# Kernel optimization log

Measured on AMD Instinct MI355X. Metric: run time of the kernel, lower is better.

Reference implementation:

```python
import jax, jax.numpy as jnp
import numpy as np

B, D, F_UP, F_DOWN, C = 4096, 768, 12288, 12288, 256


def setup_inputs() -> dict:
    key = jax.random.key(0)
    ks = jax.random.split(key, 12)
    s = np.float32(1.0 / np.sqrt(D))
    return {
        'initial_acts': jax.random.normal(ks[0], (B, D), jnp.float32),
        'x_up': jax.random.normal(ks[1], (B, D), jnp.float32),
        'ln_scale': jax.random.uniform(ks[2], (B,), jnp.float32) + 0.5,
        'W_enc_up': jax.random.normal(ks[3], (F_UP, D), jnp.float32) * s,
        'b_enc_up': jax.random.normal(ks[4], (F_UP,), jnp.float32) * 0.01,
        'b_dec_up': jax.random.normal(ks[5], (D,), jnp.float32) * 0.01,
        'W_dec_up': jax.random.normal(ks[6], (D, F_UP), jnp.float32) * s,
        'W_enc_down': jax.random.normal(ks[7], (F_DOWN, D), jnp.float32) * s,
        'b_enc_down': jax.random.normal(ks[8], (F_DOWN,), jnp.float32) * 0.01,
        'b_dec_down': jax.random.normal(ks[9], (D,), jnp.float32) * 0.01,
        'W_dec_down': jax.random.normal(ks[10], (D, F_DOWN), jnp.float32) * s,
        'connections': jax.random.randint(ks[11], (F_DOWN, C), 0, F_UP, jnp.int64),
        'k_up': 64,
        'k_down': 64,
    }


def _topk_sparse(pre, k):
    # pre: [B, F] -> keep top-k per row, zeros elsewhere
    vals, idx = jax.lax.top_k(pre, k)
    rows = jnp.arange(pre.shape[0])[:, None]
    return jnp.zeros_like(pre).at[rows, idx].set(vals)


def _topk_encode(x, W_enc, b_enc, b_dec, k):
    # AutoEncoderTopK.encode: relu(encoder(x - b_dec)), then top-k sparsify
    pre = jax.nn.relu((x - b_dec) @ W_enc.T + b_enc)
    return _topk_sparse(pre, k)


def reference(initial_acts, x_up, ln_scale, W_enc_up, b_enc_up, b_dec_up,
              W_dec_up, W_enc_down, b_enc_down, b_dec_down, W_dec_down,
              connections, k_up, k_down):
    f_down, f_up = W_enc_down.shape[0], W_enc_up.shape[0]
    # upstream features (vanilla_forward -> features[up_name])
    feat_up = _topk_encode(x_up, W_enc_up, b_enc_up, b_dec_up, k_up)  # [B, F_up]
    # connection mask [F_down, F_up] from index tensor
    rows = jnp.arange(f_down)[:, None]
    mask = jnp.zeros((f_down, f_up), jnp.bool_).at[rows, connections].set(True)
    # get_pruned_contributions: masked virtual-weight matmul
    virtual_w = (W_enc_down @ W_dec_up) * mask                        # [F_down, F_up]
    contributions = feat_up @ virtual_w.T + (W_enc_down @ b_dec_up)   # [B, F_down]
    # get_initial_contributions + accumulate
    approx = initial_acts @ W_enc_down.T + contributions
    # layernorm scale, encoder bias, b_dec correction
    approx = approx / ln_scale[:, None] + b_enc_down - (W_enc_down @ b_dec_down)
    # downstream TopK + decode
    feat_down = _topk_sparse(approx, k_down)                          # [B, F_down]
    recon = feat_down @ W_dec_down.T + b_dec_down                     # [B, D]
    return recon
```

## Files before the change

### kernel.cpp

```cpp
#include <hip/hip_runtime.h>
#include <stdint.h>

#define B_    4096
#define D_    768
#define FUP   12288
#define FDN   12288
#define CONN  256
#define KTOP  64
#define CHUNK 1024
#define NCH   (B_ / CHUNK)
#define CH2   512
#define NCH2  (B_ / CH2)
#define PDW   1024
#define NPW   (FUP / PDW)

typedef short short8v __attribute__((ext_vector_type(8)));
typedef float f32x4  __attribute__((ext_vector_type(4)));


__device__ __forceinline__ unsigned fkey(float x) {
    unsigned u = __float_as_uint(x);
    return (u & 0x80000000u) ? ~u : (u | 0x80000000u);
}

__device__ void topk64_block(const float* vals, int n, int* gidx, float* gval,
                             unsigned* hist, int* scratch)
{
    const int tid = threadIdx.x;
    const int ln = tid & 63, wv = tid >> 6;
    if (tid == 0) { scratch[0] = KTOP; scratch[1] = 0; scratch[2] = 0; scratch[3] = 0; }
    for (int l = 24; l >= 0; l -= 8) {
        hist[tid] = 0;
        __syncthreads();
        unsigned prefix = (unsigned)scratch[1];
        int need = scratch[0];
        unsigned hm = (l == 24) ? 0u : (0xFFFFFFFFu << (l + 8));
        for (int i = tid; i < n; i += 256) {
            unsigned key = fkey(vals[i]);
            if ((key & hm) == (prefix & hm)) atomicAdd(&hist[(key >> l) & 255], 1u);
        }
        __syncthreads();
        unsigned hown = hist[tid];
        unsigned x = hown;
#pragma unroll
        for (int off = 1; off < 64; off <<= 1) {
            int sl = ln + off;
            unsigned v = __shfl(x, sl < 64 ? sl : ln);
            x += (sl < 64) ? v : 0u;
        }
        if (ln == 0) ((unsigned*)scratch)[4 + wv] = x;
        __syncthreads();
        unsigned offw = 0;
        for (int w2 = wv + 1; w2 < 4; ++w2) offw += ((unsigned*)scratch)[4 + w2];
        unsigned T = x + offw;
        unsigned S = T - hown;
        if (S < (unsigned)need && T >= (unsigned)need) {
            scratch[1] = (int)(prefix | ((unsigned)tid << l));
            scratch[0] = need - (int)S;
        }
        __syncthreads();
    }
    unsigned thresh = (unsigned)scratch[1];
    for (int i = tid; i < n; i += 256) {
        float v = vals[i];
        unsigned key = fkey(v);
        if (key > thresh) {
            int p = atomicAdd(&scratch[2], 1);
            gidx[p] = i; gval[p] = v;
        } else if (key == thresh) {
            int p = atomicAdd(&scratch[3], 1);
            if (p < 64) scratch[4 + p] = i;
        }
    }
    __syncthreads();
    if (tid == 0) {
        int cnt = scratch[2];
        int ne  = KTOP - cnt;
        int ec  = scratch[3] < 64 ? scratch[3] : 64;
        for (int a2 = 0; a2 < ne; ++a2) {
            int best = 0x7fffffff, bi = -1;
            for (int q = 0; q < ec; ++q) {
                int id = scratch[4 + q];
                if (id >= 0 && id < best) { best = id; bi = q; }
            }
            if (bi >= 0) {
                scratch[4 + bi] = -1;
                gidx[cnt + a2] = best; gval[cnt + a2] = vals[best];
            }
        }
    }
    __syncthreads();
}


__global__ void k_detect(const int* __restrict__ conn, int* mode) {
    if (blockIdx.x == 0 && threadIdx.x == 0) {
        int z = 1;
        for (int i = 1; i < 128; i += 2) z &= (conn[i] == 0);
        *mode = z;
    }
}

__device__ __forceinline__ int getconn(const int* c, size_t e, int mode) {
    return mode ? c[2 * e] : c[e];
}

__global__ void k_zero(unsigned* __restrict__ p, int n) {
    for (int i = blockIdx.x * blockDim.x + threadIdx.x; i < n;
         i += gridDim.x * blockDim.x)
        p[i] = 0u;
}

__global__ void k_transpose(const float* __restrict__ in, float* __restrict__ out,
                            int R, int Cc) {
    __shared__ float t[32][33];
    int x = blockIdx.x * 32 + threadIdx.x;
    int yb = blockIdx.y * 32;
    for (int j = threadIdx.y; j < 32; j += 8)
        t[j][threadIdx.x] = in[(size_t)(yb + j) * Cc + x];
    __syncthreads();
    int xo  = yb + threadIdx.x;
    int yb2 = blockIdx.x * 32;
    for (int j = threadIdx.y; j < 32; j += 8)
        out[(size_t)(yb2 + j) * R + xo] = t[threadIdx.x][j];
}

__global__ void k_precompute(const float* __restrict__ Wup, const float* __restrict__ Wdn,
                             const float* __restrict__ b_enc_up, const float* __restrict__ b_enc_down,
                             const float* __restrict__ b_dec_up, const float* __restrict__ b_dec_down,
                             float* __restrict__ bias_up, float* __restrict__ c_in,
                             float* __restrict__ c_out) {
    int wave = threadIdx.x >> 6, lane = threadIdx.x & 63;
    int f = blockIdx.x * 4 + wave;
    if (f >= FUP) return;
    const float* ru = Wup + (size_t)f * D_;
    const float* rd = Wdn + (size_t)f * D_;
    float s1 = 0.f, s2 = 0.f, s3 = 0.f;
    for (int d = lane; d < D_; d += 64) {
        float bu = b_dec_up[d], bd = b_dec_down[d];
        s1 += ru[d] * bu;
        float w = rd[d];
        s2 += w * bu;
        s3 += w * bd;
    }
    for (int m = 32; m; m >>= 1) {
        s1 += __shfl_xor(s1, m);
        s2 += __shfl_xor(s2, m);
        s3 += __shfl_xor(s3, m);
    }
    if (!lane) {
        bias_up[f] = b_enc_up[f] - s1;
        c_in[f]  = s2;
        c_out[f] = b_enc_down[f] - s3;
    }
}

__device__ __forceinline__ unsigned short bf16rne(float f) {
    unsigned u = __float_as_uint(f);
    unsigned r = u + 0x7FFFu + ((u >> 16) & 1u);
    return (unsigned short)(r >> 16);
}
__global__ __launch_bounds__(256) void k_split3(const float* __restrict__ in,
                                                unsigned short* __restrict__ out,
                                                int R) {
    const size_t plane = (size_t)R * D_;
    size_t base = ((size_t)blockIdx.x * 256 + threadIdx.x) * 8;
    float v[8];
    *(float4*)&v[0] = *(const float4*)(in + base);
    *(float4*)&v[4] = *(const float4*)(in + base + 4);
    unsigned short h[8], m[8], l[8];
#pragma unroll
    for (int i = 0; i < 8; ++i) {
        float f = v[i];
        unsigned short hb = bf16rne(f);
        float hf = __uint_as_float((unsigned)hb << 16);
        float r1 = f - hf;
        unsigned short mb = bf16rne(r1);
        float mf = __uint_as_float((unsigned)mb << 16);
        float r2 = r1 - mf;
        unsigned short lb = bf16rne(r2);
        h[i] = hb; m[i] = mb; l[i] = lb;
    }
    *(short8v*)(out + base)             = *(short8v*)h;
    *(short8v*)(out + plane + base)     = *(short8v*)m;
    *(short8v*)(out + 2 * plane + base) = *(short8v*)l;
}

#define GBM 128
#define GBN 128
#define GBK 32

__device__ __forceinline__ void gld16(const void* g, void* l) {
    __builtin_amdgcn_global_load_lds(
        (const __attribute__((address_space(1))) unsigned int*)g,
        (__attribute__((address_space(3))) unsigned int*)l, 16, 0, 0);
}

__global__ __launch_bounds__(256, 2) void k_gemm_mfma(
    const unsigned short* __restrict__ Asp, const unsigned short* __restrict__ Bsp,
    float* __restrict__ C, const float* __restrict__ bias,
    int M, int N, int doRelu)
{
    __shared__ __attribute__((aligned(16))) unsigned short L[3072 * 8];
    const int tid = threadIdx.x;
    const int nbx = gridDim.x;
    const int nwg = nbx * gridDim.y;
    int id = blockIdx.y * nbx + blockIdx.x;
    if ((nwg & 7) == 0) id = (id & 7) * (nwg >> 3) + (id >> 3);
    const int bm = (id / nbx) * GBM, bn = (id % nbx) * GBN;

    const int wid = tid >> 6, lane = tid & 63;
    const int wm = (wid >> 1) * 64, wn = (wid & 1) * 64;
    const int l15 = lane & 15, g4 = lane >> 4;
    const size_t psA = (size_t)M * D_, psB = (size_t)N * D_;

    const unsigned short* gsrc[12];
    unsigned short* ldst[12];
#pragma unroll
    for (int q2 = 0; q2 < 12; ++q2) {
        int s  = wid * 768 + q2 * 64 + lane;
        int isB = (s >= 1536);
        int sl = isB ? (s - 1536) : s;
        int p  = sl >> 9;
        int rem = sl & 511;
        int r  = rem >> 2;
        int cs = rem & 3;
        int c  = cs ^ ((r >> 1) & 3);
        const unsigned short* bp = isB ? Bsp : Asp;
        size_t ps = isB ? psB : psA;
        int row = (isB ? bn : bm) + r;
        gsrc[q2] = bp + (size_t)p * ps + (size_t)row * D_ + c * 8;
        ldst[q2] = L + (wid * 768 + q2 * 64) * 8;
    }
    const int fA = ((wm + l15) >> 1) & 3;
    const int fB = ((wn + l15) >> 1) & 3;
    const unsigned short* aB = L + (wm + l15) * 32 + ((g4 ^ fA) * 8);
    const unsigned short* bB = L + 1536 * 8 + (wn + l15) * 32 + ((g4 ^ fB) * 8);

    f32x4 acc[4][4] = {};
    for (int k0 = 0; k0 < D_; k0 += GBK) {
        __syncthreads();
#pragma unroll
        for (int q2 = 0; q2 < 12; ++q2)
            gld16(gsrc[q2] + k0, ldst[q2]);
        __syncthreads();
        short8v af[3][4], bf[3][4];
#pragma unroll
        for (int i = 0; i < 4; ++i)
#pragma unroll
            for (int p = 0; p < 3; ++p) {
                af[p][i] = *(const short8v*)(aB + p * 4096 + i * 512);
                bf[p][i] = *(const short8v*)(bB + p * 4096 + i * 512);
            }
#pragma unroll
        for (int i = 0; i < 4; ++i)
#pragma unroll
            for (int j = 0; j < 4; ++j) {
                acc[i][j] = __builtin_amdgcn_mfma_f32_16x16x32_bf16(af[0][i], bf[0][j], acc[i][j], 0, 0, 0);
                acc[i][j] = __builtin_amdgcn_mfma_f32_16x16x32_bf16(af[0][i], bf[1][j], acc[i][j], 0, 0, 0);
                acc[i][j] = __builtin_amdgcn_mfma_f32_16x16x32_bf16(af[1][i], bf[0][j], acc[i][j], 0, 0, 0);
                acc[i][j] = __builtin_amdgcn_mfma_f32_16x16x32_bf16(af[1][i], bf[1][j], acc[i][j], 0, 0, 0);
                acc[i][j] = __builtin_amdgcn_mfma_f32_16x16x32_bf16(af[0][i], bf[2][j], acc[i][j], 0, 0, 0);
                acc[i][j] = __builtin_amdgcn_mfma_f32_16x16x32_bf16(af[2][i], bf[0][j], acc[i][j], 0, 0, 0);
            }
    }
#pragma unroll
    for (int i = 0; i < 4; ++i) {
        int gr0 = bm + wm + i * 16 + (lane >> 4) * 4;
#pragma unroll
        for (int j = 0; j < 4; ++j) {
            int gc = bn + wn + j * 16 + l15;
            float bv = bias ? bias[gc] : 0.f;
#pragma unroll
            for (int q = 0; q < 4; ++q) {
                float v = acc[i][j][q] + bv;
                if (doRelu) v = fmaxf(v, 0.f);
                C[(size_t)(gr0 + q) * N + gc] = v;
            }
        }
    }
}

__global__ __launch_bounds__(256) void k_topk_up(const float* __restrict__ big,
                                                 int* __restrict__ up_idx,
                                                 float* __restrict__ up_val) {
    __shared__ __attribute__((aligned(16))) float row[FUP];
    __shared__ unsigned hist[256];
    __shared__ int scratch[68];
    int b = blockIdx.x;
    const float4* s4 = (const float4*)(big + (size_t)b * FUP);
    float4* r4 = (float4*)row;
    for (int i = threadIdx.x; i < FUP / 4; i += 256) r4[i] = s4[i];
    __syncthreads();
    topk64_block(row, FUP, up_idx + b * 64, up_val + b * 64, hist, scratch);
}

__global__ __launch_bounds__(256) void k_sortwin(
    const int* __restrict__ conn, const int* __restrict__ mode_p,
    unsigned short* __restrict__ ent_fu, unsigned char* __restrict__ ent_c,
    unsigned short* __restrict__ woff)
{
    __shared__ int crow[CONN];
    __shared__ int cnt[NPW + 1];
    __shared__ int base[NPW + 1];
    __shared__ int cur[NPW + 1];
    int fd = blockIdx.x, tid = threadIdx.x;
    int mode = *mode_p;
    crow[tid] = getconn(conn, (size_t)fd * CONN + tid, mode);
    if (tid <= NPW) cnt[tid] = 0;
    __syncthreads();
    int fu = crow[tid];
    bool dup = false;
    for (int q = 0; q < tid; ++q) dup |= (crow[q] == fu);
    int win = dup ? NPW : (fu / PDW);
    atomicAdd(&cnt[win], 1);
    __syncthreads();
    if (tid == 0) {
        int run = 0;
        for (int i = 0; i <= NPW; ++i) { base[i] = run; run += cnt[i]; }
    }
    __syncthreads();
    if (tid <= NPW) {
        woff[fd * (NPW + 2) + tid] = (unsigned short)base[tid];
        cur[tid] = base[tid];
    }
    if (tid == 0) woff[fd * (NPW + 2) + NPW + 1] = (unsigned short)CONN;
    __syncthreads();
    int pos = atomicAdd(&cur[win], 1);
    ent_fu[(size_t)fd * CONN + pos] = (unsigned short)fu;
    ent_c[(size_t)fd * CONN + pos]  = (unsigned char)tid;
}

__global__ __launch_bounds__(256) void k_pd2(
    const float* __restrict__ Wdn, const float* __restrict__ WduT,
    const unsigned short* __restrict__ ent_fu, const unsigned char* __restrict__ ent_c,
    const unsigned short* __restrict__ woff, float* __restrict__ pd)
{
    __shared__ __attribute__((aligned(16))) float wrow[D_];
    int fd = blockIdx.x, win = blockIdx.y, tid = threadIdx.x;
    int s = woff[fd * (NPW + 2) + win];
    int e = woff[fd * (NPW + 2) + win + 1];
    if (win == NPW) {
        for (int t = s + tid; t < e; t += 256)
            pd[(size_t)fd * CONN + ent_c[(size_t)fd * CONN + t]] = 0.f;
        return;
    }
    if (s == e) return;
    const float4* wsrc = (const float4*)(Wdn + (size_t)fd * D_);
    for (int i = tid; i < D_ / 4; i += 256) ((float4*)wrow)[i] = wsrc[i];
    __syncthreads();
    const int wave = tid >> 6, lane = tid & 63;
    const int grp = lane >> 4, gi = lane & 15;
    float4 wr[12];
#pragma unroll
    for (int j = 0; j < 12; ++j)
        wr[j] = *(const float4*)&wrow[gi * 4 + j * 64];
    for (int q = s + wave * 4; q < e; q += 16) {
        int idx = q + grp;
        bool act = idx < e;
        int idxc = act ? idx : (e - 1);
        int fu = ent_fu[(size_t)fd * CONN + idxc];
        const float* wu = WduT + (size_t)fu * D_;
        float s0 = 0.f, s1 = 0.f, s2 = 0.f, s3 = 0.f;
#pragma unroll
        for (int j = 0; j < 12; j += 4) {
            float4 u0 = *(const float4*)&wu[gi * 4 + (j + 0) * 64];
            float4 u1 = *(const float4*)&wu[gi * 4 + (j + 1) * 64];
            float4 u2 = *(const float4*)&wu[gi * 4 + (j + 2) * 64];
            float4 u3 = *(const float4*)&wu[gi * 4 + (j + 3) * 64];
            s0 = fmaf(u0.x, wr[j + 0].x, s0); s0 = fmaf(u0.y, wr[j + 0].y, s0);
            s0 = fmaf(u0.z, wr[j + 0].z, s0); s0 = fmaf(u0.w, wr[j + 0].w, s0);
            s1 = fmaf(u1.x, wr[j + 1].x, s1); s1 = fmaf(u1.y, wr[j + 1].y, s1);
            s1 = fmaf(u1.z, wr[j + 1].z, s1); s1 = fmaf(u1.w, wr[j + 1].w, s1);
            s2 = fmaf(u2.x, wr[j + 2].x, s2); s2 = fmaf(u2.y, wr[j + 2].y, s2);
            s2 = fmaf(u2.z, wr[j + 2].z, s2); s2 = fmaf(u2.w, wr[j + 2].w, s2);
            s3 = fmaf(u3.x, wr[j + 3].x, s3); s3 = fmaf(u3.y, wr[j + 3].y, s3);
            s3 = fmaf(u3.z, wr[j + 3].z, s3); s3 = fmaf(u3.w, wr[j + 3].w, s3);
        }
        float sacc = (s0 + s1) + (s2 + s3);
#pragma unroll
        for (int m = 1; m < 16; m <<= 1) sacc += __shfl_xor(sacc, m);
        if (act && gi == 0)
            pd[(size_t)fd * CONN + ent_c[(size_t)fd * CONN + idx]] = sacc;
    }
}

__global__ void k_hist(const int* __restrict__ conn, const int* __restrict__ mode_p,
                       unsigned* __restrict__ counts, int total) {
    int mode = *mode_p;
    for (int e = blockIdx.x * blockDim.x + threadIdx.x; e < total;
         e += gridDim.x * blockDim.x)
        atomicAdd(&counts[getconn(conn, (size_t)e, mode)], 1u);
}

__global__ void k_scan(const unsigned* __restrict__ counts,
                       unsigned* __restrict__ offsets, unsigned* __restrict__ cursor) {
    __shared__ unsigned sums[256];
    int tid = threadIdx.x;
    const int CH = FUP / 256;
    unsigned local = 0;
    for (int i = 0; i < CH; ++i) local += counts[tid * CH + i];
    sums[tid] = local;
    __syncthreads();
    for (int off = 1; off < 256; off <<= 1) {
        unsigned v = 0;
        if (tid >= off) v = sums[tid - off];
        __syncthreads();
        sums[tid] += v;
        __syncthreads();
    }
    unsigned run = (tid == 0) ? 0u : sums[tid - 1];
    for (int i = 0; i < CH; ++i) {
        int idx = tid * CH + i;
        offsets[idx] = run;
        cursor[idx]  = run;
        run += counts[idx];
    }
    if (tid == 255) offsets[FUP] = run;
}

__global__ void k_scatter(const int* __restrict__ conn, const int* __restrict__ mode_p,
                          const float* __restrict__ pd, unsigned* __restrict__ cursor,
                          unsigned short* __restrict__ rev_fd, float* __restrict__ rev_w,
                          int total) {
    int mode = *mode_p;
    for (int e = blockIdx.x * blockDim.x + threadIdx.x; e < total;
         e += gridDim.x * blockDim.x) {
        int fu = getconn(conn, (size_t)e, mode);
        unsigned pos = atomicAdd(&cursor[fu], 1u);
        rev_fd[pos] = (unsigned short)(e >> 8);
        rev_w[pos]  = pd[e];
    }
}

__global__ __launch_bounds__(256) void k_down(
    const float* __restrict__ big , const float* __restrict__ ln_scale,
    const float* __restrict__ c_in, const float* __restrict__ c_out,
    const int* __restrict__ up_idx, const float* __restrict__ up_val,
    const unsigned* __restrict__ offsets, const unsigned short* __restrict__ rev_fd,
    const float* __restrict__ rev_w, int* __restrict__ down_idx,
    float* __restrict__ down_val)
{
    __shared__ __attribute__((aligned(16))) float contrib[FDN];
    __shared__ unsigned hist[256];
    __shared__ int scratch[68];
    int b = blockIdx.x, tid = threadIdx.x;
    float4* c4 = (float4*)contrib;
    for (int i = tid; i < FDN / 4; i += 256) c4[i] = make_float4(0.f, 0.f, 0.f, 0.f);
    __syncthreads();
    for (int j = 0; j < KTOP; ++j) {
        int fu = up_idx[b * 64 + j];
        float v = up_val[b * 64 + j];
        unsigned s = offsets[fu], e = offsets[fu + 1];
        for (unsigned t = s + tid; t < e; t += 256)
            atomicAdd(&contrib[rev_fd[t]], v * rev_w[t]);
    }
    __syncthreads();
    float ls = ln_scale[b];
    const float* ap = big + (size_t)b * FDN;
    for (int i = tid; i < FDN; i += 256)
        contrib[i] = (ap[i] + contrib[i] + c_in[i]) / ls + c_out[i];
    __syncthreads();
    topk64_block(contrib, FDN, down_idx + b * 64, down_val + b * 64, hist, scratch);
}

__global__ __launch_bounds__(256) void k_decode(
    const int* __restrict__ down_idx, const float* __restrict__ down_val,
    const float* __restrict__ WddT, const float* __restrict__ b_dec_down,
    float* __restrict__ out)
{
    __shared__ int fidx[64];
    __shared__ float fval[64];
    int b = blockIdx.x, tid = threadIdx.x;
    if (tid < 64) { fidx[tid] = down_idx[b * 64 + tid]; fval[tid] = down_val[b * 64 + tid]; }
    __syncthreads();
    float a0 = b_dec_down[tid], a1 = b_dec_down[tid + 256], a2 = b_dec_down[tid + 512];
    for (int j = 0; j < 64; ++j) {
        const float* r = WddT + (size_t)fidx[j] * D_;
        float v = fval[j];
        a0 += v * r[tid];
        a1 += v * r[tid + 256];
        a2 += v * r[tid + 512];
    }
    float* o = out + (size_t)b * D_;
    o[tid] = a0; o[tid + 256] = a1; o[tid + 512] = a2;
}


extern "C" void kernel_launch(void* const* d_in, const int* in_sizes, int n_in,
                              void* d_out, int out_size, void* d_ws, size_t ws_size,
                              hipStream_t stream)
{
    const float* initial_acts = (const float*)d_in[0];
    const float* x_up         = (const float*)d_in[1];
    const float* ln_scale     = (const float*)d_in[2];
    const float* W_enc_up     = (const float*)d_in[3];
    const float* b_enc_up     = (const float*)d_in[4];
    const float* b_dec_up     = (const float*)d_in[5];
    const float* W_dec_up     = (const float*)d_in[6];
    const float* W_enc_down   = (const float*)d_in[7];
    const float* b_enc_down   = (const float*)d_in[8];
    const float* b_dec_down   = (const float*)d_in[9];
    const float* W_dec_down   = (const float*)d_in[10];
    const int*   conn         = (const int*)d_in[11];
    float* out = (float*)d_out;

    char* w = (char*)d_ws;
    float*          big      = (float*)(w);
    float*          pd       = (float*)(w);
    unsigned short* ent_fu   = (unsigned short*)(w + 12582912);
    unsigned char*  ent_c    = (unsigned char*) (w + 18874368);
    unsigned short* woff     = (unsigned short*)(w + 22020096);
    unsigned short* Bsplit   = (unsigned short*)(w + 50331648);
    float*          Wt       = (float*)(w + 50331648);
    float*          rev_w    = (float*)(w + 106954752);
    unsigned short* Asplit1  = (unsigned short*)(w + 106954752);
    unsigned short* rev_fd   = (unsigned short*)(w + 119537664);
    unsigned short* Asplit2  = (unsigned short*)(w + 125829120);
    int*            up_idx   = (int*)  (w + 128188416);
    float*          up_val   = (float*)(w + 129236992);
    int*            down_idx = (int*)  (w + 130285568);
    float*          down_val = (float*)(w + 131334144);
    unsigned*       offsets  = (unsigned*)(w + 132382720);
    unsigned*       cursor   = (unsigned*)(w + 132448256);
    unsigned*       counts   = (unsigned*)(w + 132513792);
    float*          bias_up  = (float*)(w + 132579328);
    float*          c_in     = (float*)(w + 132628480);
    float*          c_out    = (float*)(w + 132677632);
    int*            mode_p   = (int*)  (w + 132726784);

    const int total_conn = FDN * CONN;
    dim3 tb(32, 8);

    k_detect<<<1, 64, 0, stream>>>(conn, mode_p);
    k_precompute<<<FUP / 4, 256, 0, stream>>>(W_enc_up, W_enc_down, b_enc_up, b_enc_down,
                                              b_dec_up, b_dec_down, bias_up, c_in, c_out);
    k_split3<<<FUP * D_ / 2048, 256, 0, stream>>>(W_enc_up, Bsplit, FUP);
    for (int c = 0; c < NCH; ++c) {
        k_split3<<<CHUNK * D_ / 2048, 256, 0, stream>>>(x_up + (size_t)c * CHUNK * D_,
                                                        Asplit1, CHUNK);
        k_gemm_mfma<<<dim3(FUP / GBN, CHUNK / GBM), 256, 0, stream>>>(
            Asplit1, Bsplit, big, bias_up, CHUNK, FUP, 1);
        k_topk_up<<<CHUNK, 256, 0, stream>>>(big, up_idx + (size_t)c * CHUNK * 64,
                                             up_val + (size_t)c * CHUNK * 64);
    }
    k_transpose<<<dim3(FUP / 32, D_ / 32), tb, 0, stream>>>(W_dec_up, Wt, D_, FUP);
    k_sortwin<<<FDN, 256, 0, stream>>>(conn, mode_p, ent_fu, ent_c, woff);
    k_pd2<<<dim3(FDN, NPW + 1), 256, 0, stream>>>(W_enc_down, Wt, ent_fu, ent_c, woff, pd);
    k_zero<<<48, 256, 0, stream>>>(counts, FUP);
    k_hist<<<4096, 256, 0, stream>>>(conn, mode_p, counts, total_conn);
    k_scan<<<1, 256, 0, stream>>>(counts, offsets, cursor);
    k_scatter<<<4096, 256, 0, stream>>>(conn, mode_p, pd, cursor, rev_fd, rev_w, total_conn);
    k_split3<<<FDN * D_ / 2048, 256, 0, stream>>>(W_enc_down, Bsplit, FDN);
    for (int c = 0; c < NCH2; ++c) {
        k_split3<<<CH2 * D_ / 2048, 256, 0, stream>>>(initial_acts + (size_t)c * CH2 * D_,
                                                      Asplit2, CH2);
        k_gemm_mfma<<<dim3(FDN / GBN, CH2 / GBM), 256, 0, stream>>>(
            Asplit2, Bsplit, big, nullptr, CH2, FDN, 0);
        k_down<<<CH2, 256, 0, stream>>>(big, ln_scale + (size_t)c * CH2, c_in, c_out,
                                        up_idx + (size_t)c * CH2 * 64,
                                        up_val + (size_t)c * CH2 * 64,
                                        offsets, rev_fd, rev_w,
                                        down_idx + (size_t)c * CH2 * 64,
                                        down_val + (size_t)c * CH2 * 64);
    }
    k_transpose<<<dim3(FDN / 32, D_ / 32), tb, 0, stream>>>(W_dec_down, Wt, D_, FDN);
    k_decode<<<B_, 256, 0, stream>>>(down_idx, down_val, Wt, b_dec_down, out);
}
```

Baseline: 3.325 ms.

## Fuse activation bf16x3 split into GEMM A-tile load and enlarge down chunk

The GEMM kernel now reads fp32 activations directly, splits them into three bf16 planes in registers and writes them to LDS, with register prefetch of the next K slice. This removes the separate k_split3 launches and the Asplit buffer round trips through global memory. The down-stage chunk size grows from 512 to 1024 rows, halving the number of launches. The pd dot product also loses its four-way partial sums, which lengthens the FMA dependency chain. In exchange the GEMM main loop does more VALU work per K step, and its A tile now moves through registers instead of asynchronous direct-to-LDS loads.

```diff
diff --git a/kernel.cpp b/kernel.cpp
--- a/kernel.cpp
+++ b/kernel.cpp
@@ -9,8 +9,6 @@
 #define KTOP  64
 #define CHUNK 1024
 #define NCH   (B_ / CHUNK)
-#define CH2   512
-#define NCH2  (B_ / CH2)
 #define PDW   1024
 #define NPW   (FUP / PDW)
 
@@ -196,8 +194,8 @@
         (__attribute__((address_space(3))) unsigned int*)l, 16, 0, 0);
 }
 
-__global__ __launch_bounds__(256, 2) void k_gemm_mfma(
-    const unsigned short* __restrict__ Asp, const unsigned short* __restrict__ Bsp,
+__global__ __launch_bounds__(256, 2) void k_gemm_mfma2(
+    const float* __restrict__ Afp, const unsigned short* __restrict__ Bsp,
     float* __restrict__ C, const float* __restrict__ bias,
     int M, int N, int doRelu)
 {
@@ -212,38 +210,71 @@
     const int wid = tid >> 6, lane = tid & 63;
     const int wm = (wid >> 1) * 64, wn = (wid & 1) * 64;
     const int l15 = lane & 15, g4 = lane >> 4;
-    const size_t psA = (size_t)M * D_, psB = (size_t)N * D_;
-
-    const unsigned short* gsrc[12];
-    unsigned short* ldst[12];
-#pragma unroll
-    for (int q2 = 0; q2 < 12; ++q2) {
-        int s  = wid * 768 + q2 * 64 + lane;
-        int isB = (s >= 1536);
-        int sl = isB ? (s - 1536) : s;
+    const size_t psB = (size_t)N * D_;
+
+    const unsigned short* gsrcB[6];
+    unsigned short* ldstB[6];
+#pragma unroll
+    for (int q2 = 0; q2 < 6; ++q2) {
+        int s  = 1536 + wid * 384 + q2 * 64 + lane;
+        int sl = s - 1536;
         int p  = sl >> 9;
         int rem = sl & 511;
         int r  = rem >> 2;
         int cs = rem & 3;
         int c  = cs ^ ((r >> 1) & 3);
-        const unsigned short* bp = isB ? Bsp : Asp;
-        size_t ps = isB ? psB : psA;
-        int row = (isB ? bn : bm) + r;
-        gsrc[q2] = bp + (size_t)p * ps + (size_t)row * D_ + c * 8;
-        ldst[q2] = L + (wid * 768 + q2 * 64) * 8;
-    }
+        gsrcB[q2] = Bsp + (size_t)p * psB + (size_t)(bn + r) * D_ + c * 8;
+        ldstB[q2] = L + (1536 + wid * 384 + q2 * 64) * 8;
+    }
+    const int ar = tid >> 1, ah2 = tid & 1;
+    const float* aptr = Afp + (size_t)(bm + ar) * D_ + ah2 * 16;
+    const int fR = (ar >> 1) & 3;
+    unsigned short* aw[3][2];
+#pragma unroll
+    for (int p = 0; p < 3; ++p)
+#pragma unroll
+        for (int cc = 0; cc < 2; ++cc)
+            aw[p][cc] = L + (p * 512 + ar * 4 + ((2 * ah2 + cc) ^ fR)) * 8;
+
     const int fA = ((wm + l15) >> 1) & 3;
     const int fB = ((wn + l15) >> 1) & 3;
     const unsigned short* aB = L + (wm + l15) * 32 + ((g4 ^ fA) * 8);
     const unsigned short* bB = L + 1536 * 8 + (wn + l15) * 32 + ((g4 ^ fB) * 8);
 
+    float a0[16];
+#pragma unroll
+    for (int j = 0; j < 4; ++j)
+        *(float4*)&a0[4 * j] = *(const float4*)(aptr + 4 * j);
+
     f32x4 acc[4][4] = {};
     for (int k0 = 0; k0 < D_; k0 += GBK) {
         __syncthreads();
 #pragma unroll
-        for (int q2 = 0; q2 < 12; ++q2)
-            gld16(gsrc[q2] + k0, ldst[q2]);
-        __syncthreads();
+        for (int q2 = 0; q2 < 6; ++q2)
+            gld16(gsrcB[q2] + k0, ldstB[q2]);
+        unsigned short hh_[16], mm_[16], ll_[16];
+#pragma unroll
+        for (int i = 0; i < 16; ++i) {
+            float f = a0[i];
+            unsigned short hb = bf16rne(f);
+            float hf = __uint_as_float((unsigned)hb << 16);
+            float r1 = f - hf;
+            unsigned short mb = bf16rne(r1);
+            float mf = __uint_as_float((unsigned)mb << 16);
+            unsigned short lb = bf16rne(r1 - mf);
+            hh_[i] = hb; mm_[i] = mb; ll_[i] = lb;
+        }
+#pragma unroll
+        for (int cc = 0; cc < 2; ++cc) {
+            *(short8v*)aw[0][cc] = *(const short8v*)&hh_[cc * 8];
+            *(short8v*)aw[1][cc] = *(const short8v*)&mm_[cc * 8];
+            *(short8v*)aw[2][cc] = *(const short8v*)&ll_[cc * 8];
+        }
+        __syncthreads();
+        int kn = (k0 + GBK < D_) ? (k0 + GBK) : k0;
+#pragma unroll
+        for (int j = 0; j < 4; ++j)
+            *(float4*)&a0[4 * j] = *(const float4*)(aptr + kn + 4 * j);
         short8v af[3][4], bf[3][4];
 #pragma unroll
         for (int i = 0; i < 4; ++i)
@@ -361,23 +392,15 @@
         int idxc = act ? idx : (e - 1);
         int fu = ent_fu[(size_t)fd * CONN + idxc];
         const float* wu = WduT + (size_t)fu * D_;
-        float s0 = 0.f, s1 = 0.f, s2 = 0.f, s3 = 0.f;
-#pragma unroll
-        for (int j = 0; j < 12; j += 4) {
-            float4 u0 = *(const float4*)&wu[gi * 4 + (j + 0) * 64];
-            float4 u1 = *(const float4*)&wu[gi * 4 + (j + 1) * 64];
-            float4 u2 = *(const float4*)&wu[gi * 4 + (j + 2) * 64];
-            float4 u3 = *(const float4*)&wu[gi * 4 + (j + 3) * 64];
-            s0 = fmaf(u0.x, wr[j + 0].x, s0); s0 = fmaf(u0.y, wr[j + 0].y, s0);
-            s0 = fmaf(u0.z, wr[j + 0].z, s0); s0 = fmaf(u0.w, wr[j + 0].w, s0);
-            s1 = fmaf(u1.x, wr[j + 1].x, s1); s1 = fmaf(u1.y, wr[j + 1].y, s1);
-            s1 = fmaf(u1.z, wr[j + 1].z, s1); s1 = fmaf(u1.w, wr[j + 1].w, s1);
-            s2 = fmaf(u2.x, wr[j + 2].x, s2); s2 = fmaf(u2.y, wr[j + 2].y, s2);
-            s2 = fmaf(u2.z, wr[j + 2].z, s2); s2 = fmaf(u2.w, wr[j + 2].w, s2);
-            s3 = fmaf(u3.x, wr[j + 3].x, s3); s3 = fmaf(u3.y, wr[j + 3].y, s3);
-            s3 = fmaf(u3.z, wr[j + 3].z, s3); s3 = fmaf(u3.w, wr[j + 3].w, s3);
-        }
-        float sacc = (s0 + s1) + (s2 + s3);
+        float sacc = 0.f;
+#pragma unroll
+        for (int j = 0; j < 12; ++j) {
+            float4 u = *(const float4*)&wu[gi * 4 + j * 64];
+            sacc = fmaf(u.x, wr[j].x, sacc);
+            sacc = fmaf(u.y, wr[j].y, sacc);
+            sacc = fmaf(u.z, wr[j].z, sacc);
+            sacc = fmaf(u.w, wr[j].w, sacc);
+        }
 #pragma unroll
         for (int m = 1; m < 16; m <<= 1) sacc += __shfl_xor(sacc, m);
         if (act && gi == 0)
@@ -514,20 +537,18 @@
     unsigned short* Bsplit   = (unsigned short*)(w + 50331648);
     float*          Wt       = (float*)(w + 50331648);
     float*          rev_w    = (float*)(w + 106954752);
-    unsigned short* Asplit1  = (unsigned short*)(w + 106954752);
     unsigned short* rev_fd   = (unsigned short*)(w + 119537664);
-    unsigned short* Asplit2  = (unsigned short*)(w + 125829120);
-    int*            up_idx   = (int*)  (w + 128188416);
-    float*          up_val   = (float*)(w + 129236992);
-    int*            down_idx = (int*)  (w + 130285568);
-    float*          down_val = (float*)(w + 131334144);
-    unsigned*       offsets  = (unsigned*)(w + 132382720);
-    unsigned*       cursor   = (unsigned*)(w + 132448256);
-    unsigned*       counts   = (unsigned*)(w + 132513792);
-    float*          bias_up  = (float*)(w + 132579328);
-    float*          c_in     = (float*)(w + 132628480);
-    float*          c_out    = (float*)(w + 132677632);
-    int*            mode_p   = (int*)  (w + 132726784);
+    int*            up_idx   = (int*)  (w + 125829120);
+    float*          up_val   = (float*)(w + 126877696);
+    int*            down_idx = (int*)  (w + 127926272);
+    float*          down_val = (float*)(w + 128974848);
+    unsigned*       offsets  = (unsigned*)(w + 130023424);
+    unsigned*       cursor   = (unsigned*)(w + 130088960);
+    unsigned*       counts   = (unsigned*)(w + 130154496);
+    float*          bias_up  = (float*)(w + 130220032);
+    float*          c_in     = (float*)(w + 130269184);
+    float*          c_out    = (float*)(w + 130318336);
+    int*            mode_p   = (int*)  (w + 130367488);
 
     const int total_conn = FDN * CONN;
     dim3 tb(32, 8);
@@ -537,10 +558,8 @@
                                               b_dec_up, b_dec_down, bias_up, c_in, c_out);
     k_split3<<<FUP * D_ / 2048, 256, 0, stream>>>(W_enc_up, Bsplit, FUP);
     for (int c = 0; c < NCH; ++c) {
-        k_split3<<<CHUNK * D_ / 2048, 256, 0, stream>>>(x_up + (size_t)c * CHUNK * D_,
-                                                        Asplit1, CHUNK);
-        k_gemm_mfma<<<dim3(FUP / GBN, CHUNK / GBM), 256, 0, stream>>>(
-            Asplit1, Bsplit, big, bias_up, CHUNK, FUP, 1);
+        k_gemm_mfma2<<<dim3(FUP / GBN, CHUNK / GBM), 256, 0, stream>>>(
+            x_up + (size_t)c * CHUNK * D_, Bsplit, big, bias_up, CHUNK, FUP, 1);
         k_topk_up<<<CHUNK, 256, 0, stream>>>(big, up_idx + (size_t)c * CHUNK * 64,
                                              up_val + (size_t)c * CHUNK * 64);
     }
@@ -552,17 +571,15 @@
     k_scan<<<1, 256, 0, stream>>>(counts, offsets, cursor);
     k_scatter<<<4096, 256, 0, stream>>>(conn, mode_p, pd, cursor, rev_fd, rev_w, total_conn);
     k_split3<<<FDN * D_ / 2048, 256, 0, stream>>>(W_enc_down, Bsplit, FDN);
-    for (int c = 0; c < NCH2; ++c) {
-        k_split3<<<CH2 * D_ / 2048, 256, 0, stream>>>(initial_acts + (size_t)c * CH2 * D_,
-                                                      Asplit2, CH2);
-        k_gemm_mfma<<<dim3(FDN / GBN, CH2 / GBM), 256, 0, stream>>>(
-            Asplit2, Bsplit, big, nullptr, CH2, FDN, 0);
-        k_down<<<CH2, 256, 0, stream>>>(big, ln_scale + (size_t)c * CH2, c_in, c_out,
-                                        up_idx + (size_t)c * CH2 * 64,
-                                        up_val + (size_t)c * CH2 * 64,
-                                        offsets, rev_fd, rev_w,
-                                        down_idx + (size_t)c * CH2 * 64,
-                                        down_val + (size_t)c * CH2 * 64);
+    for (int c = 0; c < NCH; ++c) {
+        k_gemm_mfma2<<<dim3(FDN / GBN, CHUNK / GBM), 256, 0, stream>>>(
+            initial_acts + (size_t)c * CHUNK * D_, Bsplit, big, nullptr, CHUNK, FDN, 0);
+        k_down<<<CHUNK, 256, 0, stream>>>(big, ln_scale + (size_t)c * CHUNK, c_in, c_out,
+                                          up_idx + (size_t)c * CHUNK * 64,
+                                          up_val + (size_t)c * CHUNK * 64,
+                                          offsets, rev_fd, rev_w,
+                                          down_idx + (size_t)c * CHUNK * 64,
+                                          down_val + (size_t)c * CHUNK * 64);
     }
     k_transpose<<<dim3(FDN / 32, D_ / 32), tb, 0, stream>>>(W_dec_down, Wt, D_, FDN);
     k_decode<<<B_, 256, 0, stream>>>(down_idx, down_val, Wt, b_dec_down, out);
```

After: 3.376 ms. No clear change (+1.5%).
